# Performance work log

Measured on AMD Instinct MI355X. Metric: run time of the kernel, lower is better.

## Reference

```python
import jax, jax.numpy as jnp
import numpy as np

WINDOW_SIZE = 11
SIGMA = 1.5
C1 = 0.01 ** 2
C2 = 0.03 ** 2
L1_WEIGHT = 1.0
SSIM_WEIGHT = 1.0


def _gaussian_window(channels, window_size=WINDOW_SIZE, sigma=SIGMA):
    x = np.arange(window_size, dtype=np.float32) - window_size // 2
    g = np.exp(-(x ** 2) / (2.0 * sigma ** 2))
    g = g / g.sum()
    w2d = np.outer(g, g).astype(np.float32)  # [ws, ws]
    # depthwise kernel layout OIHW with I=1, O=channels
    return jnp.asarray(np.tile(w2d[None, None], (channels, 1, 1, 1)))


def _dwconv(x, w):
    pad = WINDOW_SIZE // 2
    return jax.lax.conv_general_dilated(
        x, w, window_strides=(1, 1), padding=[(pad, pad), (pad, pad)],
        dimension_numbers=('NCHW', 'OIHW', 'NCHW'),
        feature_group_count=x.shape[1])


def setup_inputs() -> dict:
    key = jax.random.key(0)
    k1, k2 = jax.random.split(key)
    shape = (16, 3, 512, 512)
    outputs = jax.random.uniform(k1, shape, dtype=jnp.float32)
    labels = jax.random.uniform(k2, shape, dtype=jnp.float32)
    return {"outputs": outputs, "labels": labels}


def reference(outputs, labels):
    img1, img2 = outputs, labels
    channel = img1.shape[1]
    window = _gaussian_window(channel).astype(img1.dtype)

    mu1 = _dwconv(img1, window)
    mu2 = _dwconv(img2, window)
    mu1_sq = mu1 * mu1
    mu2_sq = mu2 * mu2
    mu1_mu2 = mu1 * mu2
    sigma1_sq = _dwconv(img1 * img1, window) - mu1_sq
    sigma2_sq = _dwconv(img2 * img2, window) - mu2_sq
    sigma12 = _dwconv(img1 * img2, window) - mu1_mu2

    ssim_map = ((2 * mu1_mu2 + C1) * (2 * sigma12 + C2)) / (
        (mu1_sq + mu2_sq + C1) * (sigma1_sq + sigma2_sq + C2))
    ssim = jnp.mean(ssim_map)

    l1_loss = jnp.mean(jnp.abs(outputs - labels))
    ssim_loss = 1.0 - ssim
    return L1_WEIGHT * l1_loss + SSIM_WEIGHT * ssim_loss
```

## Files before the change

### kernel.cpp

```cpp
#include <hip/hip_runtime.h>
#include <hip/hip_bf16.h>
#include <math.h>

#define IMG 512
#define TW 64
#define TH 32
#define NTX 8
#define NTY 16
#define NIMG 48
#define NBLOCKS (NTX * NTY * NIMG)
#define NPIX (16LL * 3 * 512 * 512)

#define C1F 0.0001f
#define C2F 0.0009f

#define SR 88

typedef __attribute__((ext_vector_type(4))) short short4v;
typedef __attribute__((ext_vector_type(8))) short short8;
typedef __attribute__((ext_vector_type(4))) float float4v;
typedef __attribute__((ext_vector_type(2))) unsigned uint2v;

__device__ __forceinline__ float4v mfma16(short4v a, short4v b, float4v c) {
#if defined(__HIP_DEVICE_COMPILE__)
    return __builtin_amdgcn_mfma_f32_16x16x16bf16_1k(a, b, c, 0, 0, 0);
#else
    return c;
#endif
}

#define GW0 0.00102838f
#define GW1 0.00759877f
#define GW2 0.03600077f
#define GW3 0.10936069f
#define GW4 0.21300539f
#define GW5 0.26601172f

__device__ __forceinline__ unsigned short f2bf(float f) {
    unsigned u = __builtin_bit_cast(unsigned, f);
    u += 0x7FFF + ((u >> 16) & 1);
    return (unsigned short)(u >> 16);
}
__device__ __forceinline__ unsigned pk2(float a, float b) {
    __hip_bfloat162 h = __float22bfloat162_rn(make_float2(a, b));
    unsigned u;
    __builtin_memcpy(&u, &h, 4);
    return u;
}

__global__ __launch_bounds__(256, 5)
void ssim_tile_kernel(const float* __restrict__ xg, const float* __restrict__ yg,
                      float* __restrict__ partials) {
    __shared__ unsigned short sbuf[2][48][SR];
    __shared__ unsigned short gwtbl[16];
    __shared__ float red[8];

    const int tid  = threadIdx.x;
    const int lane = tid & 63;
    const int w    = tid >> 6;
    const int q    = lane >> 4;
    const int n16  = lane & 15;

    const int img = blockIdx.z;
    const int r00  = blockIdx.y * TH - 5;
    const int c00a = blockIdx.x * TW - 8;
    const float* __restrict__ xi = xg + (size_t)img * (IMG * IMG);
    const float* __restrict__ yi = yg + (size_t)img * (IMG * IMG);

    if (tid < 16) {
        const float gwf[11] = {GW0, GW1, GW2, GW3, GW4, GW5, GW4, GW3, GW2, GW1, GW0};
        unsigned short v = 0;
        #pragma unroll
        for (int t = 0; t < 11; ++t)
            if (tid == t) v = f2bf(gwf[t]);
        gwtbl[tid] = v;
    }

    float l1_loc = 0.f;
    #pragma unroll
    for (int it = 0; it < 4; ++it) {
        int u = tid + it * 256;
        if (it < 3 || tid < 192) {
            int pr  = u / 20;
            int pc4 = (u - pr * 20) << 2;
            int gr = r00 + pr, gc = c00a + pc4;
            float4 xv = make_float4(0.f, 0.f, 0.f, 0.f);
            float4 yv = make_float4(0.f, 0.f, 0.f, 0.f);
            if (pr < 42 && (unsigned)gr < 512u && (unsigned)gc < 512u) {
                size_t o = (size_t)gr * IMG + gc;
                xv = *(const float4*)(xi + o);
                yv = *(const float4*)(yi + o);
            }
            *(uint2*)&sbuf[0][pr][pc4] = make_uint2(pk2(xv.x, xv.y), pk2(xv.z, xv.w));
            *(uint2*)&sbuf[1][pr][pc4] = make_uint2(pk2(yv.x, yv.y), pk2(yv.z, yv.w));
            if ((unsigned)(pr - 5) <= 31u && (unsigned)(pc4 - 8) <= 60u)
                l1_loc += fabsf(xv.x - yv.x) + fabsf(xv.y - yv.y)
                        + fabsf(xv.z - yv.z) + fabsf(xv.w - yv.w);
        }
    }
    __syncthreads();

    short8 bh;
    short4v bv0, bv1;
    {
        int baseh = q * 8 - n16 - 3;
        #pragma unroll
        for (int j = 0; j < 8; ++j)
            bh[j] = (short)gwtbl[min((unsigned)(baseh + j), 15u)];
        int base0 = q * 4 - n16, base1 = q * 4 + 16 - n16;
        #pragma unroll
        for (int j = 0; j < 4; ++j) {
            bv0[j] = (short)gwtbl[min((unsigned)(base0 + j), 15u)];
            bv1[j] = (short)gwtbl[min((unsigned)(base1 + j), 15u)];
        }
    }

    const float4v zero4 = {0.f, 0.f, 0.f, 0.f};
    uint2v d1[3][5];
    #pragma unroll
    for (int rg = 0; rg < 3; ++rg) {
        short8 ax = *(const short8*)&sbuf[0][rg * 16 + n16][w * 16 + q * 8];
        short8 ay = *(const short8*)&sbuf[1][rg * 16 + n16][w * 16 + q * 8];
        short8 axx, ayy, axy;
        {
            unsigned* px = (unsigned*)&ax;
            unsigned* py = (unsigned*)&ay;
            unsigned* pxx = (unsigned*)&axx;
            unsigned* pyy = (unsigned*)&ayy;
            unsigned* pxy = (unsigned*)&axy;
            #pragma unroll
            for (int r = 0; r < 4; ++r) {
                unsigned rx = px[r], ry = py[r];
                float xlo = __builtin_bit_cast(float, rx << 16);
                float xhi = __builtin_bit_cast(float, rx & 0xFFFF0000u);
                float ylo = __builtin_bit_cast(float, ry << 16);
                float yhi = __builtin_bit_cast(float, ry & 0xFFFF0000u);
                pxx[r] = pk2(xlo * xlo, xhi * xhi);
                pyy[r] = pk2(ylo * ylo, yhi * yhi);
                pxy[r] = pk2(xlo * ylo, xhi * yhi);
            }
        }
        float4v d;
        d = __builtin_amdgcn_mfma_f32_16x16x32_bf16(ax, bh, zero4, 0, 0, 0);
        d1[rg][0] = (uint2v){pk2(d[0], d[1]), pk2(d[2], d[3])};
        d = __builtin_amdgcn_mfma_f32_16x16x32_bf16(ay, bh, zero4, 0, 0, 0);
        d1[rg][1] = (uint2v){pk2(d[0], d[1]), pk2(d[2], d[3])};
        d = __builtin_amdgcn_mfma_f32_16x16x32_bf16(axx, bh, zero4, 0, 0, 0);
        d1[rg][2] = (uint2v){pk2(d[0], d[1]), pk2(d[2], d[3])};
        d = __builtin_amdgcn_mfma_f32_16x16x32_bf16(ayy, bh, zero4, 0, 0, 0);
        d1[rg][3] = (uint2v){pk2(d[0], d[1]), pk2(d[2], d[3])};
        d = __builtin_amdgcn_mfma_f32_16x16x32_bf16(axy, bh, zero4, 0, 0, 0);
        d1[rg][4] = (uint2v){pk2(d[0], d[1]), pk2(d[2], d[3])};
    }

    float ssim_loc = 0.f;
    #pragma unroll
    for (int rgp = 0; rgp < 2; ++rgp) {
        float4v acc5[5];
        #pragma unroll
        for (int ch = 0; ch < 5; ++ch) {
            short4v a1 = __builtin_bit_cast(short4v, d1[rgp + 1][ch]);
            short4v a0 = __builtin_bit_cast(short4v, d1[rgp][ch]);
            acc5[ch] = mfma16(a0, bv0, mfma16(a1, bv1, zero4));
        }
        #pragma unroll
        for (int r = 0; r < 4; ++r) {
            float mu1 = acc5[0][r], mu2 = acc5[1][r];
            float e11 = acc5[2][r], e22 = acc5[3][r], e12 = acc5[4][r];
            float p = mu1 * mu2;
            float s = fmaf(mu1, mu1, mu2 * mu2);
            float e = e11 + e22;
            float num1 = fmaf(2.f, p, C1F);
            float num2 = fmaf(2.f, e12 - p, C2F);
            float den1 = s + C1F;
            float den2 = (e - s) + C2F;
            ssim_loc = fmaf(num1 * num2, __builtin_amdgcn_rcpf(den1 * den2), ssim_loc);
        }
    }

    #pragma unroll
    for (int off = 32; off > 0; off >>= 1) {
        ssim_loc += __shfl_down(ssim_loc, off);
        l1_loc   += __shfl_down(l1_loc, off);
    }
    if (lane == 0) {
        red[w] = ssim_loc;
        red[4 + w] = l1_loc;
    }
    __syncthreads();
    if (tid == 0) {
        float ss = red[0] + red[1] + red[2] + red[3];
        float ll = red[4] + red[5] + red[6] + red[7];
        int bid = blockIdx.x + NTX * (blockIdx.y + NTY * blockIdx.z);
        partials[bid] = ss;
        partials[NBLOCKS + bid] = ll;
    }
}

__global__ __launch_bounds__(1024)
void finalize_kernel(const float* __restrict__ partials, float* __restrict__ out) {
    __shared__ double rs[16], rl[16];
    const int tid = threadIdx.x;
    double ss = 0.0, ll = 0.0;
    for (int i = tid; i < NBLOCKS; i += 1024) {
        ss += (double)partials[i];
        ll += (double)partials[NBLOCKS + i];
    }
    #pragma unroll
    for (int off = 32; off > 0; off >>= 1) {
        ss += __shfl_down(ss, off);
        ll += __shfl_down(ll, off);
    }
    int wave = tid >> 6, lane = tid & 63;
    if (lane == 0) { rs[wave] = ss; rl[wave] = ll; }
    __syncthreads();
    if (tid == 0) {
        double sst = 0.0, llt = 0.0;
        #pragma unroll
        for (int w = 0; w < 16; ++w) { sst += rs[w]; llt += rl[w]; }
        double invn = 1.0 / (double)NPIX;
        out[0] = (float)(llt * invn + (1.0 - sst * invn));
    }
}

extern "C" void kernel_launch(void* const* d_in, const int* in_sizes, int n_in,
                              void* d_out, int out_size, void* d_ws, size_t ws_size,
                              hipStream_t stream) {
    const float* x = (const float*)d_in[0];
    const float* y = (const float*)d_in[1];
    float* out = (float*)d_out;
    float* partials = (float*)d_ws;

    dim3 grid(NTX, NTY, NIMG);
    ssim_tile_kernel<<<grid, dim3(256), 0, stream>>>(x, y, partials);
    finalize_kernel<<<1, dim3(1024), 0, stream>>>(partials, out);
}
```

Before: 140.0 us.

## Precompute squared and cross products into shared memory during tile staging

The staging loop now loads 8 floats per thread and writes five bf16 planes (x, y, x², y², xy) into shared memory. The MFMA stage then reads each plane directly instead of recomputing the products from bf16-rounded x and y. Products are now formed from the fp32 inputs before rounding. Shared memory grows from 2×48 to 5×42 rows, so the occupancy hint drops from 5 to 4 blocks. Rows of the last row-group past 41 are clamped to stay within the smaller buffer.

```diff
diff --git a/kernel.cpp b/kernel.cpp
--- a/kernel.cpp
+++ b/kernel.cpp
@@ -14,12 +14,14 @@
 #define C1F 0.0001f
 #define C2F 0.0009f
 
+#define SROWS 42
 #define SR 88
 
 typedef __attribute__((ext_vector_type(4))) short short4v;
 typedef __attribute__((ext_vector_type(8))) short short8;
 typedef __attribute__((ext_vector_type(4))) float float4v;
 typedef __attribute__((ext_vector_type(2))) unsigned uint2v;
+typedef __attribute__((ext_vector_type(4))) unsigned uint4v;
 
 __device__ __forceinline__ float4v mfma16(short4v a, short4v b, float4v c) {
 #if defined(__HIP_DEVICE_COMPILE__)
@@ -48,10 +50,10 @@
     return u;
 }
 
-__global__ __launch_bounds__(256, 5)
+__global__ __launch_bounds__(256, 4)
 void ssim_tile_kernel(const float* __restrict__ xg, const float* __restrict__ yg,
                       float* __restrict__ partials) {
-    __shared__ unsigned short sbuf[2][48][SR];
+    __shared__ unsigned short sbuf[5][SROWS][SR];
     __shared__ unsigned short gwtbl[16];
     __shared__ float red[8];
 
@@ -78,24 +80,43 @@
 
     float l1_loc = 0.f;
     #pragma unroll
-    for (int it = 0; it < 4; ++it) {
+    for (int it = 0; it < 2; ++it) {
         int u = tid + it * 256;
-        if (it < 3 || tid < 192) {
-            int pr  = u / 20;
-            int pc4 = (u - pr * 20) << 2;
-            int gr = r00 + pr, gc = c00a + pc4;
-            float4 xv = make_float4(0.f, 0.f, 0.f, 0.f);
-            float4 yv = make_float4(0.f, 0.f, 0.f, 0.f);
-            if (pr < 42 && (unsigned)gr < 512u && (unsigned)gc < 512u) {
-                size_t o = (size_t)gr * IMG + gc;
-                xv = *(const float4*)(xi + o);
-                yv = *(const float4*)(yi + o);
+        if (it == 0 || tid < 420 - 256) {
+            int pr  = u / 10;
+            int g10 = u - pr * 10;
+            int pc8 = g10 << 3;
+            int gr = r00 + pr, gc = c00a + pc8;
+            float4 x0 = make_float4(0.f, 0.f, 0.f, 0.f), x1 = x0;
+            float4 y0 = x0, y1 = x0;
+            bool rowok = (unsigned)gr < 512u;
+            size_t o = (size_t)gr * IMG + gc;
+            if (rowok && (unsigned)gc < 512u) {
+                x0 = *(const float4*)(xi + o);
+                y0 = *(const float4*)(yi + o);
             }
-            *(uint2*)&sbuf[0][pr][pc4] = make_uint2(pk2(xv.x, xv.y), pk2(xv.z, xv.w));
-            *(uint2*)&sbuf[1][pr][pc4] = make_uint2(pk2(yv.x, yv.y), pk2(yv.z, yv.w));
-            if ((unsigned)(pr - 5) <= 31u && (unsigned)(pc4 - 8) <= 60u)
-                l1_loc += fabsf(xv.x - yv.x) + fabsf(xv.y - yv.y)
-                        + fabsf(xv.z - yv.z) + fabsf(xv.w - yv.w);
+            if (rowok && (unsigned)(gc + 4) < 512u) {
+                x1 = *(const float4*)(xi + o + 4);
+                y1 = *(const float4*)(yi + o + 4);
+            }
+            *(uint4v*)&sbuf[0][pr][pc8] = (uint4v){
+                pk2(x0.x, x0.y), pk2(x0.z, x0.w), pk2(x1.x, x1.y), pk2(x1.z, x1.w)};
+            *(uint4v*)&sbuf[1][pr][pc8] = (uint4v){
+                pk2(y0.x, y0.y), pk2(y0.z, y0.w), pk2(y1.x, y1.y), pk2(y1.z, y1.w)};
+            *(uint4v*)&sbuf[2][pr][pc8] = (uint4v){
+                pk2(x0.x * x0.x, x0.y * x0.y), pk2(x0.z * x0.z, x0.w * x0.w),
+                pk2(x1.x * x1.x, x1.y * x1.y), pk2(x1.z * x1.z, x1.w * x1.w)};
+            *(uint4v*)&sbuf[3][pr][pc8] = (uint4v){
+                pk2(y0.x * y0.x, y0.y * y0.y), pk2(y0.z * y0.z, y0.w * y0.w),
+                pk2(y1.x * y1.x, y1.y * y1.y), pk2(y1.z * y1.z, y1.w * y1.w)};
+            *(uint4v*)&sbuf[4][pr][pc8] = (uint4v){
+                pk2(x0.x * y0.x, x0.y * y0.y), pk2(x0.z * y0.z, x0.w * y0.w),
+                pk2(x1.x * y1.x, x1.y * y1.y), pk2(x1.z * y1.z, x1.w * y1.w)};
+            if ((unsigned)(pr - 5) <= 31u && (unsigned)(g10 - 1) <= 7u)
+                l1_loc += fabsf(x0.x - y0.x) + fabsf(x0.y - y0.y)
+                        + fabsf(x0.z - y0.z) + fabsf(x0.w - y0.w)
+                        + fabsf(x1.x - y1.x) + fabsf(x1.y - y1.y)
+                        + fabsf(x1.z - y1.z) + fabsf(x1.w - y1.w);
         }
     }
     __syncthreads();
@@ -119,38 +140,15 @@
     uint2v d1[3][5];
     #pragma unroll
     for (int rg = 0; rg < 3; ++rg) {
-        short8 ax = *(const short8*)&sbuf[0][rg * 16 + n16][w * 16 + q * 8];
-        short8 ay = *(const short8*)&sbuf[1][rg * 16 + n16][w * 16 + q * 8];
-        short8 axx, ayy, axy;
-        {
-            unsigned* px = (unsigned*)&ax;
-            unsigned* py = (unsigned*)&ay;
-            unsigned* pxx = (unsigned*)&axx;
-            unsigned* pyy = (unsigned*)&ayy;
-            unsigned* pxy = (unsigned*)&axy;
-            #pragma unroll
-            for (int r = 0; r < 4; ++r) {
-                unsigned rx = px[r], ry = py[r];
-                float xlo = __builtin_bit_cast(float, rx << 16);
-                float xhi = __builtin_bit_cast(float, rx & 0xFFFF0000u);
-                float ylo = __builtin_bit_cast(float, ry << 16);
-                float yhi = __builtin_bit_cast(float, ry & 0xFFFF0000u);
-                pxx[r] = pk2(xlo * xlo, xhi * xhi);
-                pyy[r] = pk2(ylo * ylo, yhi * yhi);
-                pxy[r] = pk2(xlo * ylo, xhi * yhi);
-            }
-        }
-        float4v d;
-        d = __builtin_amdgcn_mfma_f32_16x16x32_bf16(ax, bh, zero4, 0, 0, 0);
-        d1[rg][0] = (uint2v){pk2(d[0], d[1]), pk2(d[2], d[3])};
-        d = __builtin_amdgcn_mfma_f32_16x16x32_bf16(ay, bh, zero4, 0, 0, 0);
-        d1[rg][1] = (uint2v){pk2(d[0], d[1]), pk2(d[2], d[3])};
-        d = __builtin_amdgcn_mfma_f32_16x16x32_bf16(axx, bh, zero4, 0, 0, 0);
-        d1[rg][2] = (uint2v){pk2(d[0], d[1]), pk2(d[2], d[3])};
-        d = __builtin_amdgcn_mfma_f32_16x16x32_bf16(ayy, bh, zero4, 0, 0, 0);
-        d1[rg][3] = (uint2v){pk2(d[0], d[1]), pk2(d[2], d[3])};
-        d = __builtin_amdgcn_mfma_f32_16x16x32_bf16(axy, bh, zero4, 0, 0, 0);
-        d1[rg][4] = (uint2v){pk2(d[0], d[1]), pk2(d[2], d[3])};
+        int row = rg * 16 + n16;
+        if (rg == 2) row = min(row, 41);
+        const int co = w * 16 + q * 8;
+        #pragma unroll
+        for (int ch = 0; ch < 5; ++ch) {
+            short8 a = *(const short8*)&sbuf[ch][row][co];
+            float4v d = __builtin_amdgcn_mfma_f32_16x16x32_bf16(a, bh, zero4, 0, 0, 0);
+            d1[rg][ch] = (uint2v){pk2(d[0], d[1]), pk2(d[2], d[3])};
+        }
     }
 
     float ssim_loc = 0.f;
```

New measurement: 135.7 us. 1.03x faster.
